# Performance work log

Hardware: AMD Instinct MI355X
Metric: run time of the kernel (lower is better)

The kernel has to match this reference:

```python
import jax, jax.numpy as jnp
import numpy as np

SHAPE = (192, 224, 192)
COG = np.array([96.0, 112.0, 96.0], dtype=np.float32)


def _rotation(a):
    # a: (3,) angles. R = Rx @ Ry @ Rz, matching _compute_rotation.
    one = jnp.ones(()); zero = jnp.zeros(())
    cx, sx = jnp.cos(a[0]), jnp.sin(a[0])
    cy, sy = jnp.cos(a[1]), jnp.sin(a[1])
    cz, sz = jnp.cos(a[2]), jnp.sin(a[2])
    Rx = jnp.stack([jnp.stack([one, zero, zero]),
                    jnp.stack([zero, cx, -sx]),
                    jnp.stack([zero, sx, cx])])
    Ry = jnp.stack([jnp.stack([cy, zero, sy]),
                    jnp.stack([zero, one, zero]),
                    jnp.stack([-sy, zero, cy])])
    Rz = jnp.stack([jnp.stack([cz, -sz, zero]),
                    jnp.stack([sz, cz, zero]),
                    jnp.stack([zero, zero, one])])
    return Rx @ Ry @ Rz


def _compose_matrix(angle, translation, scaling, ref_v2r, flo_v2r):
    # factors are all 1; scaling param is log-scale -> exp
    ang = angle[0]
    sc = jnp.exp(scaling[0])
    tx = translation[0]
    eye = jnp.eye(4, dtype=angle.dtype)
    cog = jnp.asarray(COG, dtype=angle.dtype)
    T_center = eye.at[:3, 3].set(-cog)
    T_center_inv = eye.at[:3, 3].set(cog)
    T_sc = jnp.diag(jnp.concatenate([sc, jnp.ones((1,), angle.dtype)]))
    T_trans = eye.at[:3, 3].set(tx)
    T_rot = eye.at[:3, :3].set(_rotation(ang))
    T_rig = T_center_inv @ T_trans @ T_rot @ T_sc @ T_center
    return jnp.linalg.inv(flo_v2r) @ T_rig @ ref_v2r


def _trilinear(vol, di, dj, dk):
    # fast_3D_interp_torch, mode='linear': zero outside, clamp ceil at border
    D, H, W = vol.shape
    ok = (di > 0) & (dj > 0) & (dk > 0) & (di <= D - 1) & (dj <= H - 1) & (dk <= W - 1)
    fi = jnp.clip(jnp.floor(di), 0, D - 1)
    fj = jnp.clip(jnp.floor(dj), 0, H - 1)
    fk = jnp.clip(jnp.floor(dk), 0, W - 1)
    wi = di - fi; wj = dj - fj; wk = dk - fk
    fi = fi.astype(jnp.int32); fj = fj.astype(jnp.int32); fk = fk.astype(jnp.int32)
    ci = jnp.minimum(fi + 1, D - 1)
    cj = jnp.minimum(fj + 1, H - 1)
    ck = jnp.minimum(fk + 1, W - 1)
    c000 = vol[fi, fj, fk]; c100 = vol[ci, fj, fk]
    c010 = vol[fi, cj, fk]; c110 = vol[ci, cj, fk]
    c001 = vol[fi, fj, ck]; c101 = vol[ci, fj, ck]
    c011 = vol[fi, cj, ck]; c111 = vol[ci, cj, ck]
    out = ((c000 * (1 - wi) + c100 * wi) * (1 - wj) + (c010 * (1 - wi) + c110 * wi) * wj) * (1 - wk) \
        + ((c001 * (1 - wi) + c101 * wi) * (1 - wj) + (c011 * (1 - wi) + c111 * wi) * wj) * wk
    return jnp.where(ok, out, jnp.zeros((), vol.dtype))


def reference(image_targ, angle, translation, scaling, ref_v2r, flo_v2r):
    T = _compose_matrix(angle, translation, scaling, ref_v2r, flo_v2r)
    D, H, W = SHAPE
    ii, jj, kk = jnp.meshgrid(jnp.arange(D, dtype=image_targ.dtype),
                              jnp.arange(H, dtype=image_targ.dtype),
                              jnp.arange(W, dtype=image_targ.dtype), indexing='ij')
    di = T[0, 0] * ii + T[0, 1] * jj + T[0, 2] * kk + T[0, 3]
    dj = T[1, 0] * ii + T[1, 1] * jj + T[1, 2] * kk + T[1, 3]
    dk = T[2, 0] * ii + T[2, 1] * jj + T[2, 2] * kk + T[2, 3]
    out = _trilinear(image_targ[0, 0], di, dj, dk)
    return out[None, None]


def setup_inputs() -> dict:
    key = jax.random.key(0)
    k1, k2, k3, k4 = jax.random.split(key, 4)
    D, H, W = SHAPE
    image_targ = jax.random.normal(k1, (1, 1, D, H, W), dtype=jnp.float32)
    angle = jax.random.normal(k2, (1, 3), dtype=jnp.float32) * 0.05
    translation = jax.random.normal(k3, (1, 3), dtype=jnp.float32) * 2.0
    scaling = jax.random.normal(k4, (1, 3), dtype=jnp.float32) * 0.02
    ref_v2r = jnp.eye(4, dtype=jnp.float32)
    flo_v2r = jnp.eye(4, dtype=jnp.float32)
    return {"image_targ": image_targ, "angle": angle, "translation": translation,
            "scaling": scaling, "ref_v2r": ref_v2r, "flo_v2r": flo_v2r}
```

## Files before the change

### kernel.cpp

```cpp
#include <hip/hip_runtime.h>
#include <math.h>

#define D_DIM 192
#define H_DIM 224
#define W_DIM 192
#define TILE_ROWS 4
#define BLOCK 192
#define NUM_XCD 8
#define PBLK 2560


__device__ inline void mm4(const float* A, const float* B, float* C) {
#pragma unroll
    for (int r = 0; r < 4; ++r)
#pragma unroll
        for (int c = 0; c < 4; ++c) {
            float s = 0.f;
#pragma unroll
            for (int t = 0; t < 4; ++t) s += A[r * 4 + t] * B[t * 4 + c];
            C[r * 4 + c] = s;
        }
}

__device__ inline void inv4(const float* m, float* invOut) {
    float inv[16];
    inv[0]  =  m[5]*m[10]*m[15] - m[5]*m[11]*m[14] - m[9]*m[6]*m[15]
             + m[9]*m[7]*m[14] + m[13]*m[6]*m[11] - m[13]*m[7]*m[10];
    inv[4]  = -m[4]*m[10]*m[15] + m[4]*m[11]*m[14] + m[8]*m[6]*m[15]
             - m[8]*m[7]*m[14] - m[12]*m[6]*m[11] + m[12]*m[7]*m[10];
    inv[8]  =  m[4]*m[9]*m[15] - m[4]*m[11]*m[13] - m[8]*m[5]*m[15]
             + m[8]*m[7]*m[13] + m[12]*m[5]*m[11] - m[12]*m[7]*m[9];
    inv[12] = -m[4]*m[9]*m[14] + m[4]*m[10]*m[13] + m[8]*m[5]*m[14]
             - m[8]*m[6]*m[13] - m[12]*m[5]*m[10] + m[12]*m[6]*m[9];
    inv[1]  = -m[1]*m[10]*m[15] + m[1]*m[11]*m[14] + m[9]*m[2]*m[15]
             - m[9]*m[3]*m[14] - m[13]*m[2]*m[11] + m[13]*m[3]*m[10];
    inv[5]  =  m[0]*m[10]*m[15] - m[0]*m[11]*m[14] - m[8]*m[2]*m[15]
             + m[8]*m[3]*m[14] + m[12]*m[2]*m[11] - m[12]*m[3]*m[10];
    inv[9]  = -m[0]*m[9]*m[15] + m[0]*m[11]*m[13] + m[8]*m[1]*m[15]
             - m[8]*m[3]*m[13] - m[12]*m[1]*m[11] + m[12]*m[3]*m[9];
    inv[13] =  m[0]*m[9]*m[14] - m[0]*m[10]*m[13] - m[8]*m[1]*m[14]
             + m[8]*m[2]*m[13] + m[12]*m[1]*m[10] - m[12]*m[2]*m[9];
    inv[2]  =  m[1]*m[6]*m[15] - m[1]*m[7]*m[14] - m[5]*m[2]*m[15]
             + m[5]*m[3]*m[14] + m[13]*m[2]*m[7] - m[13]*m[3]*m[6];
    inv[6]  = -m[0]*m[6]*m[15] + m[0]*m[7]*m[14] + m[4]*m[2]*m[15]
             - m[4]*m[3]*m[14] - m[12]*m[2]*m[7] + m[12]*m[3]*m[6];
    inv[10] =  m[0]*m[5]*m[15] - m[0]*m[7]*m[13] - m[4]*m[1]*m[15]
             + m[4]*m[3]*m[13] + m[12]*m[1]*m[7] - m[12]*m[3]*m[5];
    inv[14] = -m[0]*m[5]*m[14] + m[0]*m[6]*m[13] + m[4]*m[1]*m[14]
             - m[4]*m[2]*m[13] - m[12]*m[1]*m[6] + m[12]*m[2]*m[5];
    inv[3]  = -m[1]*m[6]*m[11] + m[1]*m[7]*m[10] + m[5]*m[2]*m[11]
             - m[5]*m[3]*m[10] - m[9]*m[2]*m[7] + m[9]*m[3]*m[6];
    inv[7]  =  m[0]*m[6]*m[11] - m[0]*m[7]*m[10] - m[4]*m[2]*m[11]
             + m[4]*m[3]*m[10] + m[8]*m[2]*m[7] - m[8]*m[3]*m[6];
    inv[11] = -m[0]*m[5]*m[11] + m[0]*m[7]*m[9] + m[4]*m[1]*m[11]
             - m[4]*m[3]*m[9] - m[8]*m[1]*m[7] + m[8]*m[3]*m[5];
    inv[15] =  m[0]*m[5]*m[10] - m[0]*m[6]*m[9] - m[4]*m[1]*m[10]
             + m[4]*m[2]*m[9] + m[8]*m[1]*m[6] - m[8]*m[2]*m[5];

    float det = m[0]*inv[0] + m[1]*inv[4] + m[2]*inv[8] + m[3]*inv[12];
    det = 1.0f / det;
#pragma unroll
    for (int i = 0; i < 16; ++i) invOut[i] = inv[i] * det;
}

typedef float vf4 __attribute__((ext_vector_type(4)));
typedef float vf2 __attribute__((ext_vector_type(2)));

__device__ inline float rfl(float x) {
    return __int_as_float(__builtin_amdgcn_readfirstlane(__float_as_int(x)));
}

__global__ __launch_bounds__(BLOCK, 4) void resample_kernel(
    const float* __restrict__ vol,
    const float* __restrict__ ang,
    const float* __restrict__ tr,
    const float* __restrict__ scl,
    const float* __restrict__ ref_v2r,
    const float* __restrict__ flo_v2r,
    float* __restrict__ out) {

    constexpr int TILES_PER_I = H_DIM / TILE_ROWS;
    constexpr int NTILE_XCD = (D_DIM * TILES_PER_I) / NUM_XCD;
    constexpr int BLK_XCD = PBLK / NUM_XCD;

    __shared__ float sT[12];

    if (threadIdx.x == 0) {
        const float a0 = ang[0], a1 = ang[1], a2 = ang[2];
        const float tr0 = tr[0], tr1 = tr[1], tr2 = tr[2];
        const float sc0 = scl[0], sc1 = scl[1], sc2 = scl[2];
        vf4 refv[4], flov[4];
#pragma unroll
        for (int r = 0; r < 4; ++r) {
            refv[r] = *(const vf4*)(ref_v2r + 4 * r);
            flov[r] = *(const vf4*)(flo_v2r + 4 * r);
        }
        float refm[16], flom[16];
#pragma unroll
        for (int r = 0; r < 4; ++r)
#pragma unroll
            for (int c = 0; c < 4; ++c) {
                refm[r * 4 + c] = refv[r][c];
                flom[r * 4 + c] = flov[r][c];
            }

        const float cogx = 96.f, cogy = 112.f, cogz = 96.f;
        float cx = cosf(a0), sx = sinf(a0);
        float cy = cosf(a1), sy = sinf(a1);
        float cz = cosf(a2), sz = sinf(a2);

        float Rx[9] = {1, 0, 0, 0, cx, -sx, 0, sx, cx};
        float Ry[9] = {cy, 0, sy, 0, 1, 0, -sy, 0, cy};
        float Rz[9] = {cz, -sz, 0, sz, cz, 0, 0, 0, 1};
        float Ryz[9], R[9];
#pragma unroll
        for (int r = 0; r < 3; ++r)
#pragma unroll
            for (int c = 0; c < 3; ++c) {
                float s = 0.f;
#pragma unroll
                for (int t = 0; t < 3; ++t) s += Ry[r * 3 + t] * Rz[t * 3 + c];
                Ryz[r * 3 + c] = s;
            }
#pragma unroll
        for (int r = 0; r < 3; ++r)
#pragma unroll
            for (int c = 0; c < 3; ++c) {
                float s = 0.f;
#pragma unroll
                for (int t = 0; t < 3; ++t) s += Rx[r * 3 + t] * Ryz[t * 3 + c];
                R[r * 3 + c] = s;
            }

        float s0 = expf(sc0), s1 = expf(sc1), s2 = expf(sc2);

        float Tc[16]   = {1,0,0,-cogx, 0,1,0,-cogy, 0,0,1,-cogz, 0,0,0,1};
        float Tci[16]  = {1,0,0, cogx, 0,1,0, cogy, 0,0,1, cogz, 0,0,0,1};
        float Tsc[16]  = {s0,0,0,0, 0,s1,0,0, 0,0,s2,0, 0,0,0,1};
        float Ttr[16]  = {1,0,0,tr0, 0,1,0,tr1, 0,0,1,tr2, 0,0,0,1};
        float Trot[16] = {R[0],R[1],R[2],0, R[3],R[4],R[5],0,
                          R[6],R[7],R[8],0, 0,0,0,1};

        float m1[16], m2[16], m3[16], Trig[16];
        mm4(Tci, Ttr, m1);
        mm4(m1, Trot, m2);
        mm4(m2, Tsc, m3);
        mm4(m3, Tc, Trig);

        float floinv[16], m4v[16], T[16];
        inv4(flom, floinv);
        mm4(floinv, Trig, m4v);
        mm4(m4v, refm, T);

#pragma unroll
        for (int q = 0; q < 12; ++q) sT[q] = T[q];
    }
    __syncthreads();

    const float t00 = rfl(sT[0]),  t01 = rfl(sT[1]);
    const float t02 = rfl(sT[2]),  t03 = rfl(sT[3]);
    const float t10 = rfl(sT[4]),  t11 = rfl(sT[5]);
    const float t12 = rfl(sT[6]),  t13 = rfl(sT[7]);
    const float t20 = rfl(sT[8]),  t21 = rfl(sT[9]);
    const float t22 = rfl(sT[10]), t23 = rfl(sT[11]);

    const int b = blockIdx.x;
    const int xcd = b & (NUM_XCD - 1);
    const int q = b >> 3;
    const int k = threadIdx.x;
    const float fk = (float)k;

    for (int qq = q; qq < NTILE_XCD; qq += BLK_XCD) {
        const int sb = xcd * NTILE_XCD + qq;
        const int i = sb / TILES_PER_I;
        const int jbase = (sb - i * TILES_PER_I) * TILE_ROWS;
        const float fi = (float)i;

        vf2  p00[TILE_ROWS], p10[TILE_ROWS], p01[TILE_ROWS], p11[TILE_ROWS];
        float wi[TILE_ROWS], wj[TILE_ROWS], wk[TILE_ROWS];
        int   sel[TILE_ROWS];
        bool  okr[TILE_ROWS];

#pragma unroll
        for (int r = 0; r < TILE_ROWS; ++r) {
            const float fj = (float)(jbase + r);
            const float di = t00 * fi + t01 * fj + t02 * fk + t03;
            const float dj = t10 * fi + t11 * fj + t12 * fk + t13;
            const float dk = t20 * fi + t21 * fj + t22 * fk + t23;

            okr[r] = (di > 0.f) & (dj > 0.f) & (dk > 0.f) &
                     (di <= (float)(D_DIM - 1)) &
                     (dj <= (float)(H_DIM - 1)) &
                     (dk <= (float)(W_DIM - 1));

            float ffi = fminf(fmaxf(floorf(di), 0.f), (float)(D_DIM - 1));
            float ffj = fminf(fmaxf(floorf(dj), 0.f), (float)(H_DIM - 1));
            float ffk = fminf(fmaxf(floorf(dk), 0.f), (float)(W_DIM - 1));

            wi[r] = di - ffi; wj[r] = dj - ffj; wk[r] = dk - ffk;

            const int i0 = (int)ffi, j0 = (int)ffj, k0 = (int)ffk;
            const int i1 = min(i0 + 1, D_DIM - 1);
            const int j1 = min(j0 + 1, H_DIM - 1);
            const int koff = min(k0, W_DIM - 2);
            sel[r] = k0 - koff;

            const int base00 = (i0 * H_DIM + j0) * W_DIM + koff;
            const int base01 = (i0 * H_DIM + j1) * W_DIM + koff;
            const int base10 = (i1 * H_DIM + j0) * W_DIM + koff;
            const int base11 = (i1 * H_DIM + j1) * W_DIM + koff;

            p00[r] = *(const vf2*)(vol + base00);
            p10[r] = *(const vf2*)(vol + base10);
            p01[r] = *(const vf2*)(vol + base01);
            p11[r] = *(const vf2*)(vol + base11);
        }

        asm volatile(""
            : "+v"(p00[0]), "+v"(p10[0]), "+v"(p01[0]), "+v"(p11[0]),
              "+v"(p00[1]), "+v"(p10[1]), "+v"(p01[1]), "+v"(p11[1]),
              "+v"(p00[2]), "+v"(p10[2]), "+v"(p01[2]), "+v"(p11[2]),
              "+v"(p00[3]), "+v"(p10[3]), "+v"(p01[3]), "+v"(p11[3]));

#pragma unroll
        for (int r = 0; r < TILE_ROWS; ++r) {
            const float c000 = sel[r] ? p00[r].y : p00[r].x;
            const float c100 = sel[r] ? p10[r].y : p10[r].x;
            const float c010 = sel[r] ? p01[r].y : p01[r].x;
            const float c110 = sel[r] ? p11[r].y : p11[r].x;
            const float c001 = p00[r].y;
            const float c101 = p10[r].y;
            const float c011 = p01[r].y;
            const float c111 = p11[r].y;

            const float omwi = 1.f - wi[r], omwj = 1.f - wj[r],
                        omwk = 1.f - wk[r];
            const float val = ((c000 * omwi + c100 * wi[r]) * omwj +
                               (c010 * omwi + c110 * wi[r]) * wj[r]) * omwk +
                              ((c001 * omwi + c101 * wi[r]) * omwj +
                               (c011 * omwi + c111 * wi[r]) * wj[r]) * wk[r];
            const float res = okr[r] ? val : 0.f;
            __builtin_nontemporal_store(
                res, &out[(i * H_DIM + (jbase + r)) * W_DIM + k]);
        }
    }
}


extern "C" void kernel_launch(void* const* d_in, const int* in_sizes, int n_in,
                              void* d_out, int out_size, void* d_ws, size_t ws_size,
                              hipStream_t stream) {
    const float* image_targ  = (const float*)d_in[0];
    const float* angle       = (const float*)d_in[1];
    const float* translation = (const float*)d_in[2];
    const float* scaling     = (const float*)d_in[3];
    const float* ref_v2r     = (const float*)d_in[4];
    const float* flo_v2r     = (const float*)d_in[5];
    float* out = (float*)d_out;
    (void)d_ws; (void)ws_size;

    resample_kernel<<<PBLK, BLOCK, 0, stream>>>(image_targ, angle, translation,
                                                scaling, ref_v2r, flo_v2r, out);
}
```

Measured before the change: 116.4 us.

## Double-buffer tile gathers to overlap next tile loads with interpolation

Restructures the persistent tile loop into a two-stage software pipeline: the gathers for the next tile are issued into a second register set before the current tile is interpolated and stored. Launch bounds drop from 4 to 2 waves per SIMD so the doubled register footprint fits. The aim is to hide gather latency within each wave, at the cost of occupancy. With 2560 blocks over about 4 tiles each, the pipeline is short, so the prologue and epilogue make up a large share of the work.

```diff
diff --git a/kernel.cpp b/kernel.cpp
--- a/kernel.cpp
+++ b/kernel.cpp
@@ -70,7 +70,15 @@
     return __int_as_float(__builtin_amdgcn_readfirstlane(__float_as_int(x)));
 }
 
-__global__ __launch_bounds__(BLOCK, 4) void resample_kernel(
+struct Tile {
+    vf2  p00[TILE_ROWS], p10[TILE_ROWS], p01[TILE_ROWS], p11[TILE_ROWS];
+    float wi[TILE_ROWS], wj[TILE_ROWS], wk[TILE_ROWS];
+    int   sel[TILE_ROWS];
+    bool  okr[TILE_ROWS];
+    int   i, jbase;
+};
+
+__global__ __launch_bounds__(BLOCK, 2) void resample_kernel(
     const float* __restrict__ vol,
     const float* __restrict__ ang,
     const float* __restrict__ tr,
@@ -166,83 +174,97 @@
 
     const int b = blockIdx.x;
     const int xcd = b & (NUM_XCD - 1);
-    const int q = b >> 3;
+    const int q0 = b >> 3;
     const int k = threadIdx.x;
     const float fk = (float)k;
 
-    for (int qq = q; qq < NTILE_XCD; qq += BLK_XCD) {
+    auto load_tile = [&](int qq, Tile& t) {
         const int sb = xcd * NTILE_XCD + qq;
-        const int i = sb / TILES_PER_I;
-        const int jbase = (sb - i * TILES_PER_I) * TILE_ROWS;
-        const float fi = (float)i;
-
-        vf2  p00[TILE_ROWS], p10[TILE_ROWS], p01[TILE_ROWS], p11[TILE_ROWS];
-        float wi[TILE_ROWS], wj[TILE_ROWS], wk[TILE_ROWS];
-        int   sel[TILE_ROWS];
-        bool  okr[TILE_ROWS];
-
+        t.i = sb / TILES_PER_I;
+        t.jbase = (sb - t.i * TILES_PER_I) * TILE_ROWS;
+        const float fi = (float)t.i;
 #pragma unroll
         for (int r = 0; r < TILE_ROWS; ++r) {
-            const float fj = (float)(jbase + r);
+            const float fj = (float)(t.jbase + r);
             const float di = t00 * fi + t01 * fj + t02 * fk + t03;
             const float dj = t10 * fi + t11 * fj + t12 * fk + t13;
             const float dk = t20 * fi + t21 * fj + t22 * fk + t23;
 
-            okr[r] = (di > 0.f) & (dj > 0.f) & (dk > 0.f) &
-                     (di <= (float)(D_DIM - 1)) &
-                     (dj <= (float)(H_DIM - 1)) &
-                     (dk <= (float)(W_DIM - 1));
+            t.okr[r] = (di > 0.f) & (dj > 0.f) & (dk > 0.f) &
+                       (di <= (float)(D_DIM - 1)) &
+                       (dj <= (float)(H_DIM - 1)) &
+                       (dk <= (float)(W_DIM - 1));
 
             float ffi = fminf(fmaxf(floorf(di), 0.f), (float)(D_DIM - 1));
             float ffj = fminf(fmaxf(floorf(dj), 0.f), (float)(H_DIM - 1));
             float ffk = fminf(fmaxf(floorf(dk), 0.f), (float)(W_DIM - 1));
 
-            wi[r] = di - ffi; wj[r] = dj - ffj; wk[r] = dk - ffk;
+            t.wi[r] = di - ffi; t.wj[r] = dj - ffj; t.wk[r] = dk - ffk;
 
             const int i0 = (int)ffi, j0 = (int)ffj, k0 = (int)ffk;
             const int i1 = min(i0 + 1, D_DIM - 1);
             const int j1 = min(j0 + 1, H_DIM - 1);
             const int koff = min(k0, W_DIM - 2);
-            sel[r] = k0 - koff;
+            t.sel[r] = k0 - koff;
 
             const int base00 = (i0 * H_DIM + j0) * W_DIM + koff;
             const int base01 = (i0 * H_DIM + j1) * W_DIM + koff;
             const int base10 = (i1 * H_DIM + j0) * W_DIM + koff;
             const int base11 = (i1 * H_DIM + j1) * W_DIM + koff;
 
-            p00[r] = *(const vf2*)(vol + base00);
-            p10[r] = *(const vf2*)(vol + base10);
-            p01[r] = *(const vf2*)(vol + base01);
-            p11[r] = *(const vf2*)(vol + base11);
-        }
-
+            t.p00[r] = *(const vf2*)(vol + base00);
+            t.p10[r] = *(const vf2*)(vol + base10);
+            t.p01[r] = *(const vf2*)(vol + base01);
+            t.p11[r] = *(const vf2*)(vol + base11);
+        }
+    };
+
+    auto consume_tile = [&](Tile& t) {
         asm volatile(""
-            : "+v"(p00[0]), "+v"(p10[0]), "+v"(p01[0]), "+v"(p11[0]),
-              "+v"(p00[1]), "+v"(p10[1]), "+v"(p01[1]), "+v"(p11[1]),
-              "+v"(p00[2]), "+v"(p10[2]), "+v"(p01[2]), "+v"(p11[2]),
-              "+v"(p00[3]), "+v"(p10[3]), "+v"(p01[3]), "+v"(p11[3]));
-
+            : "+v"(t.p00[0]), "+v"(t.p10[0]), "+v"(t.p01[0]), "+v"(t.p11[0]),
+              "+v"(t.p00[1]), "+v"(t.p10[1]), "+v"(t.p01[1]), "+v"(t.p11[1]),
+              "+v"(t.p00[2]), "+v"(t.p10[2]), "+v"(t.p01[2]), "+v"(t.p11[2]),
+              "+v"(t.p00[3]), "+v"(t.p10[3]), "+v"(t.p01[3]), "+v"(t.p11[3])
+            :
+            : "memory");
 #pragma unroll
         for (int r = 0; r < TILE_ROWS; ++r) {
-            const float c000 = sel[r] ? p00[r].y : p00[r].x;
-            const float c100 = sel[r] ? p10[r].y : p10[r].x;
-            const float c010 = sel[r] ? p01[r].y : p01[r].x;
-            const float c110 = sel[r] ? p11[r].y : p11[r].x;
-            const float c001 = p00[r].y;
-            const float c101 = p10[r].y;
-            const float c011 = p01[r].y;
-            const float c111 = p11[r].y;
-
-            const float omwi = 1.f - wi[r], omwj = 1.f - wj[r],
-                        omwk = 1.f - wk[r];
-            const float val = ((c000 * omwi + c100 * wi[r]) * omwj +
-                               (c010 * omwi + c110 * wi[r]) * wj[r]) * omwk +
-                              ((c001 * omwi + c101 * wi[r]) * omwj +
-                               (c011 * omwi + c111 * wi[r]) * wj[r]) * wk[r];
-            const float res = okr[r] ? val : 0.f;
+            const float c000 = t.sel[r] ? t.p00[r].y : t.p00[r].x;
+            const float c100 = t.sel[r] ? t.p10[r].y : t.p10[r].x;
+            const float c010 = t.sel[r] ? t.p01[r].y : t.p01[r].x;
+            const float c110 = t.sel[r] ? t.p11[r].y : t.p11[r].x;
+            const float c001 = t.p00[r].y;
+            const float c101 = t.p10[r].y;
+            const float c011 = t.p01[r].y;
+            const float c111 = t.p11[r].y;
+
+            const float omwi = 1.f - t.wi[r], omwj = 1.f - t.wj[r],
+                        omwk = 1.f - t.wk[r];
+            const float val = ((c000 * omwi + c100 * t.wi[r]) * omwj +
+                               (c010 * omwi + c110 * t.wi[r]) * t.wj[r]) * omwk +
+                              ((c001 * omwi + c101 * t.wi[r]) * omwj +
+                               (c011 * omwi + c111 * t.wi[r]) * t.wj[r]) * t.wk[r];
+            const float res = t.okr[r] ? val : 0.f;
             __builtin_nontemporal_store(
-                res, &out[(i * H_DIM + (jbase + r)) * W_DIM + k]);
-        }
+                res, &out[(t.i * H_DIM + (t.jbase + r)) * W_DIM + k]);
+        }
+    };
+
+    Tile A, B;
+    int qq = q0;
+    load_tile(qq, A);
+    int nq = qq + BLK_XCD;
+    while (true) {
+        const bool hnB = (nq < NTILE_XCD);
+        if (hnB) load_tile(nq, B);
+        consume_tile(A);
+        if (!hnB) break;
+        nq += BLK_XCD;
+        const bool hnA = (nq < NTILE_XCD);
+        if (hnA) load_tile(nq, A);
+        consume_tile(B);
+        if (!hnA) break;
+        nq += BLK_XCD;
     }
 }
 
```

After: 115.1 us. About the same (-1.1%).

## Replace persistent grid-stride loop with one 8-row tile per block

Applied to the files above, without the earlier changes.

Drops the persistent grid of 2560 blocks that looped over tiles and instead launches one block per 8-row tile (5376 blocks), still mapping blocks to XCDs in contiguous chunks. Each thread now issues 32 gathers up front instead of 16, for more memory-level parallelism. Address computation is simplified to one base plus i/j offsets. The cost is that every block recomputes the 4x4 matrix composition and inverse on thread 0, 5376 times in total, and the doubled in-flight gathers raise register pressure.

```diff
diff --git a/kernel.cpp b/kernel.cpp
--- a/kernel.cpp
+++ b/kernel.cpp
@@ -4,10 +4,9 @@
 #define D_DIM 192
 #define H_DIM 224
 #define W_DIM 192
-#define TILE_ROWS 4
+#define TILE_ROWS 8
 #define BLOCK 192
 #define NUM_XCD 8
-#define PBLK 2560
 
 
 __device__ inline void mm4(const float* A, const float* B, float* C) {
@@ -80,8 +79,8 @@
     float* __restrict__ out) {
 
     constexpr int TILES_PER_I = H_DIM / TILE_ROWS;
-    constexpr int NTILE_XCD = (D_DIM * TILES_PER_I) / NUM_XCD;
-    constexpr int BLK_XCD = PBLK / NUM_XCD;
+    constexpr int NBLK = D_DIM * TILES_PER_I;
+    constexpr int PER_XCD = NBLK / NUM_XCD;
 
     __shared__ float sT[12];
 
@@ -167,82 +166,82 @@
     const int b = blockIdx.x;
     const int xcd = b & (NUM_XCD - 1);
     const int q = b >> 3;
+    const int sb = xcd * PER_XCD + q;
+    const int i = sb / TILES_PER_I;
+    const int jbase = (sb - i * TILES_PER_I) * TILE_ROWS;
     const int k = threadIdx.x;
+
+    const float fi = (float)i;
     const float fk = (float)k;
 
-    for (int qq = q; qq < NTILE_XCD; qq += BLK_XCD) {
-        const int sb = xcd * NTILE_XCD + qq;
-        const int i = sb / TILES_PER_I;
-        const int jbase = (sb - i * TILES_PER_I) * TILE_ROWS;
-        const float fi = (float)i;
-
-        vf2  p00[TILE_ROWS], p10[TILE_ROWS], p01[TILE_ROWS], p11[TILE_ROWS];
-        float wi[TILE_ROWS], wj[TILE_ROWS], wk[TILE_ROWS];
-        int   sel[TILE_ROWS];
-        bool  okr[TILE_ROWS];
-
-#pragma unroll
-        for (int r = 0; r < TILE_ROWS; ++r) {
-            const float fj = (float)(jbase + r);
-            const float di = t00 * fi + t01 * fj + t02 * fk + t03;
-            const float dj = t10 * fi + t11 * fj + t12 * fk + t13;
-            const float dk = t20 * fi + t21 * fj + t22 * fk + t23;
-
-            okr[r] = (di > 0.f) & (dj > 0.f) & (dk > 0.f) &
-                     (di <= (float)(D_DIM - 1)) &
-                     (dj <= (float)(H_DIM - 1)) &
-                     (dk <= (float)(W_DIM - 1));
-
-            float ffi = fminf(fmaxf(floorf(di), 0.f), (float)(D_DIM - 1));
-            float ffj = fminf(fmaxf(floorf(dj), 0.f), (float)(H_DIM - 1));
-            float ffk = fminf(fmaxf(floorf(dk), 0.f), (float)(W_DIM - 1));
-
-            wi[r] = di - ffi; wj[r] = dj - ffj; wk[r] = dk - ffk;
-
-            const int i0 = (int)ffi, j0 = (int)ffj, k0 = (int)ffk;
-            const int i1 = min(i0 + 1, D_DIM - 1);
-            const int j1 = min(j0 + 1, H_DIM - 1);
-            const int koff = min(k0, W_DIM - 2);
-            sel[r] = k0 - koff;
-
-            const int base00 = (i0 * H_DIM + j0) * W_DIM + koff;
-            const int base01 = (i0 * H_DIM + j1) * W_DIM + koff;
-            const int base10 = (i1 * H_DIM + j0) * W_DIM + koff;
-            const int base11 = (i1 * H_DIM + j1) * W_DIM + koff;
-
-            p00[r] = *(const vf2*)(vol + base00);
-            p10[r] = *(const vf2*)(vol + base10);
-            p01[r] = *(const vf2*)(vol + base01);
-            p11[r] = *(const vf2*)(vol + base11);
-        }
-
-        asm volatile(""
-            : "+v"(p00[0]), "+v"(p10[0]), "+v"(p01[0]), "+v"(p11[0]),
-              "+v"(p00[1]), "+v"(p10[1]), "+v"(p01[1]), "+v"(p11[1]),
-              "+v"(p00[2]), "+v"(p10[2]), "+v"(p01[2]), "+v"(p11[2]),
-              "+v"(p00[3]), "+v"(p10[3]), "+v"(p01[3]), "+v"(p11[3]));
-
-#pragma unroll
-        for (int r = 0; r < TILE_ROWS; ++r) {
-            const float c000 = sel[r] ? p00[r].y : p00[r].x;
-            const float c100 = sel[r] ? p10[r].y : p10[r].x;
-            const float c010 = sel[r] ? p01[r].y : p01[r].x;
-            const float c110 = sel[r] ? p11[r].y : p11[r].x;
-            const float c001 = p00[r].y;
-            const float c101 = p10[r].y;
-            const float c011 = p01[r].y;
-            const float c111 = p11[r].y;
-
-            const float omwi = 1.f - wi[r], omwj = 1.f - wj[r],
-                        omwk = 1.f - wk[r];
-            const float val = ((c000 * omwi + c100 * wi[r]) * omwj +
-                               (c010 * omwi + c110 * wi[r]) * wj[r]) * omwk +
-                              ((c001 * omwi + c101 * wi[r]) * omwj +
-                               (c011 * omwi + c111 * wi[r]) * wj[r]) * wk[r];
-            const float res = okr[r] ? val : 0.f;
-            __builtin_nontemporal_store(
-                res, &out[(i * H_DIM + (jbase + r)) * W_DIM + k]);
-        }
+    vf2  p00[TILE_ROWS], p10[TILE_ROWS], p01[TILE_ROWS], p11[TILE_ROWS];
+    float wi[TILE_ROWS], wj[TILE_ROWS], wk[TILE_ROWS];
+    int   sel[TILE_ROWS];
+    bool  okr[TILE_ROWS];
+
+#pragma unroll
+    for (int r = 0; r < TILE_ROWS; ++r) {
+        const float fj = (float)(jbase + r);
+        const float di = t00 * fi + t01 * fj + t02 * fk + t03;
+        const float dj = t10 * fi + t11 * fj + t12 * fk + t13;
+        const float dk = t20 * fi + t21 * fj + t22 * fk + t23;
+
+        okr[r] = (di > 0.f) & (dj > 0.f) & (dk > 0.f) &
+                 (di <= (float)(D_DIM - 1)) &
+                 (dj <= (float)(H_DIM - 1)) &
+                 (dk <= (float)(W_DIM - 1));
+
+        float ffi = fminf(fmaxf(floorf(di), 0.f), (float)(D_DIM - 1));
+        float ffj = fminf(fmaxf(floorf(dj), 0.f), (float)(H_DIM - 1));
+        float ffk = fminf(fmaxf(floorf(dk), 0.f), (float)(W_DIM - 1));
+
+        wi[r] = di - ffi; wj[r] = dj - ffj; wk[r] = dk - ffk;
+
+        const int i0 = (int)ffi, j0 = (int)ffj, k0 = (int)ffk;
+        const int i1 = min(i0 + 1, D_DIM - 1);
+        const int j1 = min(j0 + 1, H_DIM - 1);
+        const int koff = min(k0, W_DIM - 2);
+        sel[r] = k0 - koff;
+
+        const int base00 = (i0 * H_DIM + j0) * W_DIM + koff;
+        const int dj_off = (j1 - j0) * W_DIM;
+        const int di_off = (i1 - i0) * (H_DIM * W_DIM);
+
+        p00[r] = *(const vf2*)(vol + base00);
+        p10[r] = *(const vf2*)(vol + base00 + di_off);
+        p01[r] = *(const vf2*)(vol + base00 + dj_off);
+        p11[r] = *(const vf2*)(vol + base00 + di_off + dj_off);
+    }
+
+    asm volatile(""
+        : "+v"(p00[0]), "+v"(p10[0]), "+v"(p01[0]), "+v"(p11[0]),
+          "+v"(p00[1]), "+v"(p10[1]), "+v"(p01[1]), "+v"(p11[1]),
+          "+v"(p00[2]), "+v"(p10[2]), "+v"(p01[2]), "+v"(p11[2]),
+          "+v"(p00[3]), "+v"(p10[3]), "+v"(p01[3]), "+v"(p11[3]));
+    asm volatile(""
+        : "+v"(p00[4]), "+v"(p10[4]), "+v"(p01[4]), "+v"(p11[4]),
+          "+v"(p00[5]), "+v"(p10[5]), "+v"(p01[5]), "+v"(p11[5]),
+          "+v"(p00[6]), "+v"(p10[6]), "+v"(p01[6]), "+v"(p11[6]),
+          "+v"(p00[7]), "+v"(p10[7]), "+v"(p01[7]), "+v"(p11[7]));
+
+#pragma unroll
+    for (int r = 0; r < TILE_ROWS; ++r) {
+        const float c000 = sel[r] ? p00[r].y : p00[r].x;
+        const float c100 = sel[r] ? p10[r].y : p10[r].x;
+        const float c010 = sel[r] ? p01[r].y : p01[r].x;
+        const float c110 = sel[r] ? p11[r].y : p11[r].x;
+        const float c001 = p00[r].y;
+        const float c101 = p10[r].y;
+        const float c011 = p01[r].y;
+        const float c111 = p11[r].y;
+
+        const float omwi = 1.f - wi[r], omwj = 1.f - wj[r], omwk = 1.f - wk[r];
+        const float val = ((c000 * omwi + c100 * wi[r]) * omwj +
+                           (c010 * omwi + c110 * wi[r]) * wj[r]) * omwk +
+                          ((c001 * omwi + c101 * wi[r]) * omwj +
+                           (c011 * omwi + c111 * wi[r]) * wj[r]) * wk[r];
+        const float res = okr[r] ? val : 0.f;
+        __builtin_nontemporal_store(res, &out[(i * H_DIM + (jbase + r)) * W_DIM + k]);
     }
 }
 
@@ -259,6 +258,7 @@
     float* out = (float*)d_out;
     (void)d_ws; (void)ws_size;
 
-    resample_kernel<<<PBLK, BLOCK, 0, stream>>>(image_targ, angle, translation,
+    const int nblk = D_DIM * (H_DIM / TILE_ROWS);
+    resample_kernel<<<nblk, BLOCK, 0, stream>>>(image_targ, angle, translation,
                                                 scaling, ref_v2r, flo_v2r, out);
 }
```

Measured after the change: 116.0 us. No clear change (-0.3%).
